# Performance work log

Hardware: AMD Instinct MI355X
Metric: run time of the kernel (lower is better)

## Reference

```python
import jax, jax.numpy as jnp
import numpy as np
from jax import lax

CHANNELS = 3
SCALE = 0.25
SIGMA = (1.0 / SCALE - 1.0) / 2.0          # 1.5
KSIZE = 2 * round(SIGMA * 4) + 1           # 13
KA = KSIZE // 2                            # 6 (symmetric since KSIZE odd)
KB = KA


def _gaussian_kernel():
    # separable 2D gaussian, normalized to sum 1, shape [K, K, 1, C] (HWIO, depthwise)
    r = jnp.arange(KSIZE, dtype=jnp.float32)
    mean = (KSIZE - 1) / 2.0
    g1d = jnp.exp(-((r - mean) ** 2) / (2.0 * SIGMA ** 2))
    k2d = g1d[:, None] * g1d[None, :]
    k2d = k2d / jnp.sum(k2d)
    return jnp.tile(k2d[:, :, None, None], (1, 1, 1, CHANNELS))


def setup_inputs() -> dict:
    key = jax.random.key(0)
    x = jax.random.normal(key, (32, 512, 512, CHANNELS), dtype=jnp.float32)
    return {"x": x}


def reference(x) -> jnp.ndarray:
    N, H, W, C = x.shape
    kernel = _gaussian_kernel()
    # depthwise gaussian blur; symmetric (ka, kb) zero padding + VALID == SAME output size
    blurred = lax.conv_general_dilated(
        x, kernel,
        window_strides=(1, 1),
        padding=((KA, KB), (KA, KB)),
        dimension_numbers=("NHWC", "HWIO", "NHWC"),
        feature_group_count=C,
    )
    # nearest-neighbor downsample: src = min(floor(dst * in/out), in-1)
    y_max = int(H * SCALE)
    x_max = int(W * SCALE)
    ys = jnp.minimum(jnp.floor(jnp.arange(y_max, dtype=jnp.float32) * (H / y_max)), H - 1).astype(jnp.int32)
    xs = jnp.minimum(jnp.floor(jnp.arange(x_max, dtype=jnp.float32) * (W / x_max)), W - 1).astype(jnp.int32)
    return blurred[:, ys][:, :, xs]  # [N, y_max, x_max, C]
```

## Files before the change

### kernel.cpp

```cpp
#include <hip/hip_runtime.h>
#include <math.h>


namespace {
constexpr int N_IMG   = 32;
constexpr int H_IN    = 512;
constexpr int W_IN    = 512;
constexpr int C_CH    = 3;
constexpr int H_OUT   = 128;
constexpr int W_OUT   = 128;
constexpr int T_ROWS  = 8;
constexpr int BANDS   = H_OUT / T_ROWS;
constexpr int PITCH   = 532;
constexpr int ROW_ELEMS = W_IN * C_CH;
constexpr int NTHREADS = 384;
constexpr int LDS_FLOATS = 2 * 3 * PITCH;
}

__device__ __forceinline__ float4 f4fma(float w, const float4& p, const float4& a) {
  return make_float4(fmaf(w, p.x, a.x), fmaf(w, p.y, a.y),
                     fmaf(w, p.z, a.z), fmaf(w, p.w, a.w));
}

__global__ __launch_bounds__(NTHREADS, 2)
void aa_blur_down(const float* __restrict__ in, float* __restrict__ out) {
  __shared__ __align__(16) float lds[LDS_FLOATS];

  const int tid = threadIdx.x;
  const int j   = tid / 3;
  const int c   = tid % 3;
  const int n    = blockIdx.x / BANDS;
  const int band = blockIdx.x % BANDS;
  const int i0   = band * T_ROWS;

  float wt[13];
  {
    float s = 0.f;
#pragma unroll
    for (int r = 0; r < 13; ++r) {
      const float d = (float)r - 6.0f;
      wt[r] = expf(-d * d * (1.0f / 4.5f));
      s += wt[r];
    }
    const float inv = 1.0f / s;
#pragma unroll
    for (int r = 0; r < 13; ++r) wt[r] *= inv;
  }

  const int qstart = i0 - 2;
  const float* img = in + (size_t)n * H_IN * ROW_ELEMS;

  for (int idx = tid; idx < LDS_FLOATS; idx += NTHREADS) lds[idx] = 0.f;
  __syncthreads();

  int off_e[4];
#pragma unroll
  for (int e = 0; e < 4; ++e) {
    const int ce = c + e;
    const int cc = (ce >= 3) ? ce - 3 : ce;
    const int xx = (4 * tid) / 3 + ((ce >= 3) ? 1 : 0);
    off_e[e] = cc * PITCH + xx + 8;
  }

  float4 P[3][4];
  auto loadq = [&](int slot, int s) {
    const int q = qstart + s;
#pragma unroll
    for (int m = 0; m < 4; ++m) {
      const bool dead = (s == 0 && m < 2) || (s == 10 && m == 3);
      const int y = 4 * q + m;
      if (!dead && (unsigned)y < (unsigned)H_IN) {
        P[slot][m] = reinterpret_cast<const float4*>(img + (size_t)y * ROW_ELEMS)[tid];
      } else {
        P[slot][m] = make_float4(0.f, 0.f, 0.f, 0.f);
      }
    }
  };

  float4 A0 = make_float4(0,0,0,0), A1 = A0, A2 = A0, A3 = A0;

  loadq(0, 0);
  loadq(1, 1);

#pragma unroll
  for (int s = 0; s <= 10; ++s) {
    if (s + 2 <= 10) loadq((s + 2) % 3, s + 2);

    const float4 p0 = P[s % 3][0];
    const float4 p1 = P[s % 3][1];
    const float4 p2 = P[s % 3][2];
    const float4 p3 = P[s % 3][3];

    if (s >= 3)           { A0 = f4fma(wt[10], p0, A0); A0 = f4fma(wt[11], p1, A0); A0 = f4fma(wt[12], p2, A0); }
    if (s >= 2 && s <= 9) { A1 = f4fma(wt[6],  p0, A1); A1 = f4fma(wt[7],  p1, A1); A1 = f4fma(wt[8],  p2, A1); A1 = f4fma(wt[9], p3, A1); }
    if (s >= 1 && s <= 8) { A2 = f4fma(wt[2],  p0, A2); A2 = f4fma(wt[3],  p1, A2); A2 = f4fma(wt[4],  p2, A2); A2 = f4fma(wt[5], p3, A2); }
    if (s <= 7)           { A3 = f4fma(wt[0],  p2, A3); A3 = f4fma(wt[1],  p3, A3); }

    if (s >= 3) {
      const int i = i0 + s - 3;
      const int b = (s - 3) & 1;
      float* buf = &lds[b * 3 * PITCH];
      buf[off_e[0]] = A0.x;
      buf[off_e[1]] = A0.y;
      buf[off_e[2]] = A0.z;
      buf[off_e[3]] = A0.w;
      __syncthreads();

      const float4* pl = reinterpret_cast<const float4*>(&buf[c * PITCH + 4 * j]);
      const float4 wa = pl[0];
      const float4 wb = pl[1];
      const float4 wc = pl[2];
      const float4 wd = pl[3];
      float hh;
      hh = wt[0] * wa.z;
      hh = fmaf(wt[1],  wa.w, hh);
      hh = fmaf(wt[2],  wb.x, hh);
      hh = fmaf(wt[3],  wb.y, hh);
      hh = fmaf(wt[4],  wb.z, hh);
      hh = fmaf(wt[5],  wb.w, hh);
      hh = fmaf(wt[6],  wc.x, hh);
      hh = fmaf(wt[7],  wc.y, hh);
      hh = fmaf(wt[8],  wc.z, hh);
      hh = fmaf(wt[9],  wc.w, hh);
      hh = fmaf(wt[10], wd.x, hh);
      hh = fmaf(wt[11], wd.y, hh);
      hh = fmaf(wt[12], wd.z, hh);
      out[(size_t)(n * H_OUT + i) * (W_OUT * C_CH) + tid] = hh;
    }

    A0 = A1; A1 = A2; A2 = A3; A3 = make_float4(0.f, 0.f, 0.f, 0.f);
  }
}

extern "C" void kernel_launch(void* const* d_in, const int* in_sizes, int n_in,
                              void* d_out, int out_size, void* d_ws, size_t ws_size,
                              hipStream_t stream) {
  const float* x = (const float*)d_in[0];
  float* out = (float*)d_out;
  (void)in_sizes; (void)n_in; (void)out_size; (void)d_ws; (void)ws_size;
  hipLaunchKernelGGL(aa_blur_down, dim3(N_IMG * BANDS), dim3(NTHREADS), 0, stream, x, out);
}
```

Baseline: 147.8 us.

## Split row band into per-wave column segments to remove block barriers

Each wave now handles a 16-output-column segment of a band, with its own LDS slice holding the halo. This lets the horizontal pass sync with only a wave-local lgkmcnt wait instead of __syncthreads. The grid grows by splitting each band into two 256-thread blocks, and occupancy targets 3 blocks per CU. The cost is redundant halo loads for overlapping columns, plus lanes idle during the horizontal pass (only 48 of 64 are active).

```diff
diff --git a/kernel.cpp b/kernel.cpp
--- a/kernel.cpp
+++ b/kernel.cpp
@@ -11,10 +11,15 @@
 constexpr int W_OUT   = 128;
 constexpr int T_ROWS  = 8;
 constexpr int BANDS   = H_OUT / T_ROWS;
-constexpr int PITCH   = 532;
 constexpr int ROW_ELEMS = W_IN * C_CH;
-constexpr int NTHREADS = 384;
-constexpr int LDS_FLOATS = 2 * 3 * PITCH;
+constexpr int WAVES   = 4;
+constexpr int NTHREADS = 64 * WAVES;
+constexpr int SEG_COLS = 16;
+constexpr int BLOCKS_PER_BAND = (W_OUT / SEG_COLS) / WAVES;
+constexpr int SEGC    = 76;
+constexpr int SEGPAD  = 232;
+constexpr int LDS_PER_WAVE = 2 * SEGPAD;
+constexpr int LDS_FLOATS   = WAVES * LDS_PER_WAVE;
 }
 
 __device__ __forceinline__ float4 f4fma(float w, const float4& p, const float4& a) {
@@ -22,16 +27,20 @@
                      fmaf(w, p.z, a.z), fmaf(w, p.w, a.w));
 }
 
-__global__ __launch_bounds__(NTHREADS, 2)
+__global__ __launch_bounds__(NTHREADS, 3)
 void aa_blur_down(const float* __restrict__ in, float* __restrict__ out) {
   __shared__ __align__(16) float lds[LDS_FLOATS];
 
-  const int tid = threadIdx.x;
-  const int j   = tid / 3;
-  const int c   = tid % 3;
-  const int n    = blockIdx.x / BANDS;
-  const int band = blockIdx.x % BANDS;
+  const int tid  = threadIdx.x;
+  const int lane = tid & 63;
+  const int wv   = tid >> 6;
+  const int bid  = blockIdx.x;
+  const int n    = bid / (BANDS * BLOCKS_PER_BAND);
+  const int rr   = bid % (BANDS * BLOCKS_PER_BAND);
+  const int band = rr / BLOCKS_PER_BAND;
+  const int half = rr % BLOCKS_PER_BAND;
   const int i0   = band * T_ROWS;
+  const int j0   = (half * WAVES + wv) * SEG_COLS;
 
   float wt[13];
   {
@@ -47,30 +56,37 @@
     for (int r = 0; r < 13; ++r) wt[r] *= inv;
   }
 
+  float* const wlds = &lds[wv * LDS_PER_WAVE];
+  for (int idx = lane; idx < LDS_PER_WAVE; idx += 64) wlds[idx] = 0.f;
+  asm volatile("s_waitcnt lgkmcnt(0)" ::: "memory");
+
+  const int g = 12 * j0 - 20 + 4 * lane;
+  const bool vload = (g >= 0) && (g < ROW_ELEMS);
+  int offs[4];
+#pragma unroll
+  for (int e = 0; e < 4; ++e) {
+    const int gg  = (vload ? g : 0) + e;
+    const int cc  = gg % 3;
+    const int xx  = gg / 3;
+    const int rel = xx - (4 * j0 - 6);
+    offs[e] = (rel >= 0 && rel < SEGC) ? (cc * SEGC + rel) : (3 * SEGC);
+  }
+
   const int qstart = i0 - 2;
   const float* img = in + (size_t)n * H_IN * ROW_ELEMS;
 
-  for (int idx = tid; idx < LDS_FLOATS; idx += NTHREADS) lds[idx] = 0.f;
-  __syncthreads();
-
-  int off_e[4];
-#pragma unroll
-  for (int e = 0; e < 4; ++e) {
-    const int ce = c + e;
-    const int cc = (ce >= 3) ? ce - 3 : ce;
-    const int xx = (4 * tid) / 3 + ((ce >= 3) ? 1 : 0);
-    off_e[e] = cc * PITCH + xx + 8;
-  }
+  const int  jr   = lane / 3;
+  const int  ch   = lane % 3;
+  const bool hact = (lane < 48);
 
   float4 P[3][4];
   auto loadq = [&](int slot, int s) {
-    const int q = qstart + s;
 #pragma unroll
     for (int m = 0; m < 4; ++m) {
       const bool dead = (s == 0 && m < 2) || (s == 10 && m == 3);
-      const int y = 4 * q + m;
-      if (!dead && (unsigned)y < (unsigned)H_IN) {
-        P[slot][m] = reinterpret_cast<const float4*>(img + (size_t)y * ROW_ELEMS)[tid];
+      const int y = 4 * (qstart + s) + m;
+      if (!dead && vload && (unsigned)y < (unsigned)H_IN) {
+        P[slot][m] = *reinterpret_cast<const float4*>(img + (size_t)y * ROW_ELEMS + g);
       } else {
         P[slot][m] = make_float4(0.f, 0.f, 0.f, 0.f);
       }
@@ -98,34 +114,34 @@
 
     if (s >= 3) {
       const int i = i0 + s - 3;
-      const int b = (s - 3) & 1;
-      float* buf = &lds[b * 3 * PITCH];
-      buf[off_e[0]] = A0.x;
-      buf[off_e[1]] = A0.y;
-      buf[off_e[2]] = A0.z;
-      buf[off_e[3]] = A0.w;
-      __syncthreads();
-
-      const float4* pl = reinterpret_cast<const float4*>(&buf[c * PITCH + 4 * j]);
-      const float4 wa = pl[0];
-      const float4 wb = pl[1];
-      const float4 wc = pl[2];
-      const float4 wd = pl[3];
-      float hh;
-      hh = wt[0] * wa.z;
-      hh = fmaf(wt[1],  wa.w, hh);
-      hh = fmaf(wt[2],  wb.x, hh);
-      hh = fmaf(wt[3],  wb.y, hh);
-      hh = fmaf(wt[4],  wb.z, hh);
-      hh = fmaf(wt[5],  wb.w, hh);
-      hh = fmaf(wt[6],  wc.x, hh);
-      hh = fmaf(wt[7],  wc.y, hh);
-      hh = fmaf(wt[8],  wc.z, hh);
-      hh = fmaf(wt[9],  wc.w, hh);
-      hh = fmaf(wt[10], wd.x, hh);
-      hh = fmaf(wt[11], wd.y, hh);
-      hh = fmaf(wt[12], wd.z, hh);
-      out[(size_t)(n * H_OUT + i) * (W_OUT * C_CH) + tid] = hh;
+      float* buf = wlds + ((s - 3) & 1) * SEGPAD;
+      if (vload) {
+        buf[offs[0]] = A0.x; buf[offs[1]] = A0.y;
+        buf[offs[2]] = A0.z; buf[offs[3]] = A0.w;
+      }
+      asm volatile("s_waitcnt lgkmcnt(0)" ::: "memory");
+      if (hact) {
+        const float* pl = buf + ch * SEGC + 4 * jr;
+        const float4 wa = *reinterpret_cast<const float4*>(pl);
+        const float4 wb = *reinterpret_cast<const float4*>(pl + 4);
+        const float4 wc = *reinterpret_cast<const float4*>(pl + 8);
+        const float  wd = pl[12];
+        float hh;
+        hh = wt[0] * wa.x;
+        hh = fmaf(wt[1],  wa.y, hh);
+        hh = fmaf(wt[2],  wa.z, hh);
+        hh = fmaf(wt[3],  wa.w, hh);
+        hh = fmaf(wt[4],  wb.x, hh);
+        hh = fmaf(wt[5],  wb.y, hh);
+        hh = fmaf(wt[6],  wb.z, hh);
+        hh = fmaf(wt[7],  wb.w, hh);
+        hh = fmaf(wt[8],  wc.x, hh);
+        hh = fmaf(wt[9],  wc.y, hh);
+        hh = fmaf(wt[10], wc.z, hh);
+        hh = fmaf(wt[11], wc.w, hh);
+        hh = fmaf(wt[12], wd,   hh);
+        out[(size_t)(n * H_OUT + i) * (W_OUT * C_CH) + 3 * j0 + lane] = hh;
+      }
     }
 
     A0 = A1; A1 = A2; A2 = A3; A3 = make_float4(0.f, 0.f, 0.f, 0.f);
@@ -136,7 +152,8 @@
                               void* d_out, int out_size, void* d_ws, size_t ws_size,
                               hipStream_t stream) {
   const float* x = (const float*)d_in[0];
-  float* out = (float*)d_out;
+  float* outp = (float*)d_out;
   (void)in_sizes; (void)n_in; (void)out_size; (void)d_ws; (void)ws_size;
-  hipLaunchKernelGGL(aa_blur_down, dim3(N_IMG * BANDS), dim3(NTHREADS), 0, stream, x, out);
+  hipLaunchKernelGGL(aa_blur_down, dim3(N_IMG * BANDS * BLOCKS_PER_BAND),
+                     dim3(NTHREADS), 0, stream, x, outp);
 }
```

Result: no change. 147.2 us (-0.4%).
